# Kernel optimization log

Measured on AMD Instinct MI355X. Metric: run time of the kernel, lower is better.

## Reference

```python
import jax, jax.numpy as jnp
import numpy as np

N_BLADES = 8  # Cl(3,0): 1, e1, e2, e3 and their products (bitmask blade indexing)


def _blade_sign(a: int, b: int) -> int:
    # Sign from reordering basis vectors when multiplying blades a*b (Euclidean metric).
    a >>= 1
    s = 0
    while a:
        s += bin(a & b).count('1')
        a >>= 1
    return -1 if (s & 1) else 1


def make_cayley() -> np.ndarray:
    C = np.zeros((N_BLADES, N_BLADES, N_BLADES), dtype=np.float32)
    for a in range(N_BLADES):
        for b in range(N_BLADES):
            C[a, b, a ^ b] = float(_blade_sign(a, b))
    return C


def setup_inputs() -> dict:
    key = jax.random.key(0)
    k1, k2 = jax.random.split(key)
    B, Cin, Cout = 8192, 256, 256
    scale = 1.0 / np.sqrt(Cin * N_BLADES)
    x = jax.random.normal(k1, (B, Cin, N_BLADES), dtype=jnp.float32)
    weight = jax.random.normal(k2, (Cout, Cin, N_BLADES), dtype=jnp.float32) * scale
    bias = jnp.zeros((Cout, N_BLADES), dtype=jnp.float32)
    cayley = jnp.asarray(make_cayley())
    return {"x": x, "weight": weight, "bias": bias, "cayley": cayley}


def reference(x, weight, bias, cayley):
    # A[b,o,j,k] = sum_i W[o,i,j] * X[b,i,k]  (weight blade j times input blade k)
    A = jnp.einsum('oij,bik->bojk', weight, x)
    # Contract blade pair (j,k) into output blade l via sparse Cayley table.
    out = jnp.einsum('jkl,bojk->bol', cayley, A)
    return out + bias[None, :, :]
```

## Files before the change

kernel.cpp:

```cpp
#include <hip/hip_runtime.h>
#include <stdint.h>
#include <stddef.h>


typedef __bf16 bf16x8  __attribute__((ext_vector_type(8)));
typedef float  f32x4   __attribute__((ext_vector_type(4)));

#define BM 256
#define BN 256
#define KSLICE 32
#define NSLICES 64
#define SLOT_ELEMS (256 * 32)

__device__ __forceinline__ void async_copy16(void* lds_dst, const void* g_src) {
    __builtin_amdgcn_global_load_lds(
        (__attribute__((address_space(1))) void*)g_src,
        (__attribute__((address_space(3))) void*)lds_dst,
        16, 0, 0);
}

__global__ __launch_bounds__(256) void prep_kernel(
    const float* __restrict__ x, __bf16* __restrict__ Xb, long nx,
    const float* __restrict__ W, const float* __restrict__ cayley,
    __bf16* __restrict__ Wt, int Cin, int Cout, int castBlocks)
{
    __shared__ float Cay[512];
    if ((int)blockIdx.x < castBlocks) {
        long i = ((long)blockIdx.x * 256 + threadIdx.x) * 8;
        if (i + 8 <= nx) {
            const f32x4* p = (const f32x4*)(x + i);
            f32x4 v0 = p[0];
            f32x4 v1 = p[1];
            bf16x8 o;
            o[0] = (__bf16)v0[0]; o[1] = (__bf16)v0[1];
            o[2] = (__bf16)v0[2]; o[3] = (__bf16)v0[3];
            o[4] = (__bf16)v1[0]; o[5] = (__bf16)v1[1];
            o[6] = (__bf16)v1[2]; o[7] = (__bf16)v1[3];
            *(bf16x8*)(Xb + i) = o;
        }
        return;
    }
    for (int t = threadIdx.x; t < 512; t += 256) Cay[t] = cayley[t];
    __syncthreads();

    int flat = (blockIdx.x - castBlocks) * 256 + threadIdx.x;
    int total = Cout * 8 * Cin;
    if (flat >= total) return;
    int i = flat % Cin;
    int n = flat / Cin;
    int o = n >> 3, l = n & 7;

    const float* wrow = W + ((size_t)o * Cin + i) * 8;
    float w8[8];
    #pragma unroll
    for (int j = 0; j < 8; ++j) w8[j] = wrow[j];

    bf16x8 outv;
    #pragma unroll
    for (int k = 0; k < 8; ++k) {
        float s = 0.f;
        #pragma unroll
        for (int j = 0; j < 8; ++j) s += Cay[j * 64 + k * 8 + l] * w8[j];
        outv[k] = (__bf16)s;
    }
    *(bf16x8*)(Wt + (size_t)n * (Cin * 8) + i * 8) = outv;
}

__global__ __launch_bounds__(512, 2) void gemm_bt_kernel(
    const __bf16* __restrict__ A,
    const __bf16* __restrict__ Bt,
    const float*  __restrict__ bias,
    float* __restrict__ C,
    int M, int N, int K)
{
    __shared__ __align__(16) __bf16 As[4][SLOT_ELEMS];
    __shared__ __align__(16) __bf16 Bs[4][SLOT_ELEMS];

    const int tid  = threadIdx.x;
    const int wave = tid >> 6;
    const int lane = tid & 63;
    const int quad = lane >> 4;
    const int l16  = lane & 15;

    const int bid = blockIdx.x;
    const int xcd = bid & 7;
    const int idx = bid >> 3;
    const int mBase = (xcd * 4 + (idx & 3)) * BM;
    const int nBase = (idx >> 2) * BN;

    const int srow = lane >> 2;
    const int sgrp = (lane & 3) ^ ((lane >> 3) & 3);
    const __bf16* gA0 = A  + (size_t)(mBase + wave * 32 +  0 + srow) * K + sgrp * 8;
    const __bf16* gA1 = A  + (size_t)(mBase + wave * 32 + 16 + srow) * K + sgrp * 8;
    const __bf16* gB0 = Bt + (size_t)(nBase + wave * 32 +  0 + srow) * K + sgrp * 8;
    const __bf16* gB1 = Bt + (size_t)(nBase + wave * 32 + 16 + srow) * K + sgrp * 8;
    const int stOff = wave * 1024;

#define STAGE_A(slot, q) do {                                          \
        async_copy16(&As[slot][stOff      ], gA0 + (size_t)(q) * KSLICE); \
        async_copy16(&As[slot][stOff + 512], gA1 + (size_t)(q) * KSLICE); \
    } while (0)
#define STAGE_B(slot, q) do {                                          \
        async_copy16(&Bs[slot][stOff      ], gB0 + (size_t)(q) * KSLICE); \
        async_copy16(&Bs[slot][stOff + 512], gB1 + (size_t)(q) * KSLICE); \
    } while (0)

    const int wm = wave >> 2;
    const int wn = wave & 3;
    const int offq = (quad ^ ((l16 >> 1) & 3)) * 8;
    const int aOff = (wm * 128 + l16) * KSLICE + offq;
    const int bOff = (wn * 64  + l16) * KSLICE + offq;

    f32x4 acc[8][4] = {};

    STAGE_A(0, 0); STAGE_B(0, 0);
    STAGE_A(1, 1); STAGE_B(1, 1);
    STAGE_A(2, 2); STAGE_B(2, 2);
    STAGE_B(3, 3);
    asm volatile("s_waitcnt vmcnt(6)" ::: "memory");
    __syncthreads();

    #pragma unroll 2
    for (int s = 0; s < NSLICES; ++s) {
        const __bf16* pa = &As[s & 3][aOff];
        const __bf16* pb = &Bs[s & 3][bOff];

        bf16x8 af0[4], bf[4];
        #pragma unroll
        for (int j = 0; j < 4; ++j) af0[j] = *(const bf16x8*)(pa + j * 512);
        #pragma unroll
        for (int n = 0; n < 4; ++n) bf[n]  = *(const bf16x8*)(pb + n * 512);
        if (s <= 60) STAGE_A((s + 3) & 3, s + 3);
        __builtin_amdgcn_s_barrier();
        asm volatile("s_waitcnt lgkmcnt(0)" ::: "memory");
        __builtin_amdgcn_s_setprio(1);
        #pragma unroll
        for (int j = 0; j < 4; ++j)
            #pragma unroll
            for (int n = 0; n < 4; ++n)
                acc[j][n] = __builtin_amdgcn_mfma_f32_16x16x32_bf16(
                    af0[j], bf[n], acc[j][n], 0, 0, 0);
        __builtin_amdgcn_s_setprio(0);
        __builtin_amdgcn_s_barrier();

        bf16x8 af1[4];
        #pragma unroll
        for (int j = 0; j < 4; ++j) af1[j] = *(const bf16x8*)(pa + (4 + j) * 512);
        if (s <= 59) STAGE_B(s & 3, s + 4);
        __builtin_amdgcn_s_barrier();
        asm volatile("s_waitcnt lgkmcnt(0)" ::: "memory");
        __builtin_amdgcn_s_setprio(1);
        #pragma unroll
        for (int j = 0; j < 4; ++j)
            #pragma unroll
            for (int n = 0; n < 4; ++n)
                acc[4 + j][n] = __builtin_amdgcn_mfma_f32_16x16x32_bf16(
                    af1[j], bf[n], acc[4 + j][n], 0, 0, 0);
        __builtin_amdgcn_s_setprio(0);
        if (s & 1) {
            if (s >= 61) asm volatile("s_waitcnt vmcnt(0)" ::: "memory");
            else         asm volatile("s_waitcnt vmcnt(6)" ::: "memory");
        }
        __builtin_amdgcn_s_barrier();
    }

#undef STAGE_A
#undef STAGE_B

    float bv[4];
    #pragma unroll
    for (int n = 0; n < 4; ++n)
        bv[n] = bias[nBase + wn * 64 + n * 16 + l16];

    #pragma unroll
    for (int m = 0; m < 8; ++m) {
        #pragma unroll
        for (int n = 0; n < 4; ++n) {
            const int col = nBase + wn * 64 + n * 16 + l16;
            #pragma unroll
            for (int r = 0; r < 4; ++r) {
                const int row = mBase + wm * 128 + m * 16 + quad * 4 + r;
                C[(size_t)row * N + col] = acc[m][n][r] + bv[n];
            }
        }
    }
}

extern "C" void kernel_launch(void* const* d_in, const int* in_sizes, int n_in,
                              void* d_out, int out_size, void* d_ws, size_t ws_size,
                              hipStream_t stream) {
    const float* x      = (const float*)d_in[0];
    const float* weight = (const float*)d_in[1];
    const float* bias   = (const float*)d_in[2];
    const float* cayley = (const float*)d_in[3];
    float* out = (float*)d_out;

    const int Cout = in_sizes[2] / 8;
    const int Cin  = in_sizes[1] / (Cout * 8);
    const int Bm   = in_sizes[0] / (Cin * 8);
    const int M = Bm;
    const int N = Cout * 8;
    const int K = Cin * 8;

    __bf16* Xb = (__bf16*)d_ws;
    __bf16* Wt = (__bf16*)((char*)d_ws + (size_t)M * K * 2);

    long nx = (long)M * K;
    int castBlocks = (int)(nx / 8 / 256);
    int foldBlocks = (N * Cin + 255) / 256;
    prep_kernel<<<castBlocks + foldBlocks, 256, 0, stream>>>(
        x, Xb, nx, weight, cayley, Wt, Cin, Cout, castBlocks);

    int grid = (M / BM) * (N / BN);
    gemm_bt_kernel<<<grid, 512, 0, stream>>>(Xb, Wt, bias, out, M, N, K);
}
```

Measured before the change: 178.7 us.

## Software-pipeline LDS fragment loads with register double-buffering in GEMM main loop

Restructures the GEMM k-loop into a manually unrolled four-slice body. The next slice's A and B fragments are loaded from LDS into alternate register sets while the current slice's second MFMA half runs. This removes one barrier and one lgkmcnt wait per slice and aims to hide LDS latency behind MFMA work. The cost is more registers, and the hand-set vmcnt thresholds in the peeled tail are easy to get wrong, which risks reading LDS slots before their loads finish.

```diff
diff --git a/kernel.cpp b/kernel.cpp
--- a/kernel.cpp
+++ b/kernel.cpp
@@ -96,11 +96,11 @@
     const __bf16* gB1 = Bt + (size_t)(nBase + wave * 32 + 16 + srow) * K + sgrp * 8;
     const int stOff = wave * 1024;
 
-#define STAGE_A(slot, q) do {                                          \
+#define STAGE_A(slot, q) do {                                             \
         async_copy16(&As[slot][stOff      ], gA0 + (size_t)(q) * KSLICE); \
         async_copy16(&As[slot][stOff + 512], gA1 + (size_t)(q) * KSLICE); \
     } while (0)
-#define STAGE_B(slot, q) do {                                          \
+#define STAGE_B(slot, q) do {                                             \
         async_copy16(&Bs[slot][stOff      ], gB0 + (size_t)(q) * KSLICE); \
         async_copy16(&Bs[slot][stOff + 512], gB1 + (size_t)(q) * KSLICE); \
     } while (0)
@@ -108,62 +108,77 @@
     const int wm = wave >> 2;
     const int wn = wave & 3;
     const int offq = (quad ^ ((l16 >> 1) & 3)) * 8;
-    const int aOff = (wm * 128 + l16) * KSLICE + offq;
-    const int bOff = (wn * 64  + l16) * KSLICE + offq;
+    const __bf16* paBase = &As[0][(wm * 128 + l16) * KSLICE + offq];
+    const __bf16* pbBase = &Bs[0][(wn * 64  + l16) * KSLICE + offq];
 
     f32x4 acc[8][4] = {};
+    bf16x8 af0A[4], bfA[4], af0B[4], bfB[4], af1[4];
 
     STAGE_A(0, 0); STAGE_B(0, 0);
     STAGE_A(1, 1); STAGE_B(1, 1);
     STAGE_A(2, 2); STAGE_B(2, 2);
     STAGE_B(3, 3);
-    asm volatile("s_waitcnt vmcnt(6)" ::: "memory");
-    __syncthreads();
-
-    #pragma unroll 2
-    for (int s = 0; s < NSLICES; ++s) {
-        const __bf16* pa = &As[s & 3][aOff];
-        const __bf16* pb = &Bs[s & 3][bOff];
-
-        bf16x8 af0[4], bf[4];
-        #pragma unroll
-        for (int j = 0; j < 4; ++j) af0[j] = *(const bf16x8*)(pa + j * 512);
-        #pragma unroll
-        for (int n = 0; n < 4; ++n) bf[n]  = *(const bf16x8*)(pb + n * 512);
-        if (s <= 60) STAGE_A((s + 3) & 3, s + 3);
-        __builtin_amdgcn_s_barrier();
-        asm volatile("s_waitcnt lgkmcnt(0)" ::: "memory");
-        __builtin_amdgcn_s_setprio(1);
-        #pragma unroll
-        for (int j = 0; j < 4; ++j)
-            #pragma unroll
-            for (int n = 0; n < 4; ++n)
-                acc[j][n] = __builtin_amdgcn_mfma_f32_16x16x32_bf16(
-                    af0[j], bf[n], acc[j][n], 0, 0, 0);
-        __builtin_amdgcn_s_setprio(0);
-        __builtin_amdgcn_s_barrier();
-
-        bf16x8 af1[4];
-        #pragma unroll
-        for (int j = 0; j < 4; ++j) af1[j] = *(const bf16x8*)(pa + (4 + j) * 512);
-        if (s <= 59) STAGE_B(s & 3, s + 4);
-        __builtin_amdgcn_s_barrier();
-        asm volatile("s_waitcnt lgkmcnt(0)" ::: "memory");
-        __builtin_amdgcn_s_setprio(1);
-        #pragma unroll
-        for (int j = 0; j < 4; ++j)
-            #pragma unroll
-            for (int n = 0; n < 4; ++n)
-                acc[4 + j][n] = __builtin_amdgcn_mfma_f32_16x16x32_bf16(
-                    af1[j], bf[n], acc[4 + j][n], 0, 0, 0);
-        __builtin_amdgcn_s_setprio(0);
-        if (s & 1) {
-            if (s >= 61) asm volatile("s_waitcnt vmcnt(0)" ::: "memory");
-            else         asm volatile("s_waitcnt vmcnt(6)" ::: "memory");
-        }
-        __builtin_amdgcn_s_barrier();
-    }
-
+    asm volatile("s_waitcnt vmcnt(10)" ::: "memory");
+    __builtin_amdgcn_s_barrier();
+
+    #pragma unroll
+    for (int j = 0; j < 4; ++j)
+        af0A[j] = *(const bf16x8*)(paBase + j * 512);
+    #pragma unroll
+    for (int j = 0; j < 4; ++j)
+        bfA[j]  = *(const bf16x8*)(pbBase + j * 512);
+
+#define SLICE_BODY(s_, c_, n_, AF0, BF, NAF0, NBF, DOA, DOB, DOPF)             \
+    do {                                                                       \
+        _Pragma("unroll")                                                      \
+        for (int j = 0; j < 4; ++j)                                            \
+            af1[j] = *(const bf16x8*)(paBase + (c_) * SLOT_ELEMS + (4 + j) * 512); \
+        if (DOA) STAGE_A(((s_) + 3) & 3, (s_) + 3);                            \
+        __builtin_amdgcn_s_setprio(1);                                         \
+        _Pragma("unroll")                                                      \
+        for (int j = 0; j < 4; ++j)                                            \
+            _Pragma("unroll")                                                  \
+            for (int n = 0; n < 4; ++n)                                        \
+                acc[j][n] = __builtin_amdgcn_mfma_f32_16x16x32_bf16(           \
+                    AF0[j], BF[n], acc[j][n], 0, 0, 0);                        \
+        __builtin_amdgcn_s_setprio(0);                                         \
+        asm volatile("s_waitcnt vmcnt(8)" ::: "memory");                       \
+        __builtin_amdgcn_s_barrier();                                          \
+        if (DOPF) {                                                            \
+            _Pragma("unroll")                                                  \
+            for (int j = 0; j < 4; ++j)                                        \
+                NAF0[j] = *(const bf16x8*)(paBase + (n_) * SLOT_ELEMS + j * 512); \
+            _Pragma("unroll")                                                  \
+            for (int j = 0; j < 4; ++j)                                        \
+                NBF[j] = *(const bf16x8*)(pbBase + (n_) * SLOT_ELEMS + j * 512); \
+        }                                                                      \
+        if (DOB) STAGE_B((s_) & 3, (s_) + 4);                                  \
+        __builtin_amdgcn_s_setprio(1);                                         \
+        _Pragma("unroll")                                                      \
+        for (int j = 0; j < 4; ++j)                                            \
+            _Pragma("unroll")                                                  \
+            for (int n = 0; n < 4; ++n)                                        \
+                acc[4 + j][n] = __builtin_amdgcn_mfma_f32_16x16x32_bf16(       \
+                    af1[j], BF[n], acc[4 + j][n], 0, 0, 0);                    \
+        __builtin_amdgcn_s_setprio(0);                                         \
+        __builtin_amdgcn_s_barrier();                                          \
+    } while (0)
+
+    #pragma unroll 1
+    for (int s4 = 0; s4 < 15; ++s4) {
+        const int s = s4 * 4;
+        SLICE_BODY(s + 0, 0, 1, af0A, bfA, af0B, bfB, true, true, true);
+        SLICE_BODY(s + 1, 1, 2, af0B, bfB, af0A, bfA, true, true, true);
+        SLICE_BODY(s + 2, 2, 3, af0A, bfA, af0B, bfB, true, true, true);
+        SLICE_BODY(s + 3, 3, 0, af0B, bfB, af0A, bfA, true, true, true);
+    }
+    SLICE_BODY(60, 0, 1, af0A, bfA, af0B, bfB, true,  false, true);
+    SLICE_BODY(61, 1, 2, af0B, bfB, af0A, bfA, false, false, true);
+    SLICE_BODY(62, 2, 3, af0A, bfA, af0B, bfB, false, false, true);
+    SLICE_BODY(63, 3, 0, af0B, bfB, af0A, bfA, false, false, false);
+    asm volatile("s_waitcnt vmcnt(0)" ::: "memory");
+
+#undef SLICE_BODY
 #undef STAGE_A
 #undef STAGE_B
 
```

Result: no change. 176.4 us (-1.3%).
